# Optimization experiments

Measured on AMD Instinct MI355X. Metric: run time of the kernel, lower is better.

## Reference

```python
import jax, jax.numpy as jnp
import numpy as np

T, B, I, H = 512, 64, 1024, 1024


def setup_inputs() -> dict:
    key = jax.random.key(0)
    ks = jax.random.split(key, 5)
    s = 1.0 / np.sqrt(H)  # torch Linear default init scale
    return {
        "X": jax.random.normal(ks[0], (T, B, I), dtype=jnp.float32),
        "Wi": jax.random.uniform(ks[1], (4, H, I), dtype=jnp.float32, minval=-s, maxval=s),
        "Wh": jax.random.uniform(ks[2], (4, H, H), dtype=jnp.float32, minval=-s, maxval=s),
        "bi": jax.random.uniform(ks[3], (4, H), dtype=jnp.float32, minval=-s, maxval=s),
        "bh": jax.random.uniform(ks[4], (4, H), dtype=jnp.float32, minval=-s, maxval=s),
    }


def _lstm(X, Wi, Wh, bi, bh):
    # Precompute input projections for all timesteps: [T, 4, B, H]
    Gx = jnp.einsum('tbi,ghi->tgbh', X, Wi) + (bi + bh)[None, :, None, :]

    def step(carry, gx):
        h, c = carry
        g = gx + jnp.einsum('ghk,bk->gbh', Wh, h)  # [4, B, H]
        f = jax.nn.sigmoid(g[0])
        i = jax.nn.sigmoid(g[1])
        gg = jnp.tanh(g[2])
        c = f * c + i * gg
        o = jax.nn.sigmoid(g[3])
        h = o * jnp.tanh(c)
        return (h, c), h

    h0 = jnp.zeros((B, H), dtype=X.dtype)
    c0 = jnp.zeros((B, H), dtype=X.dtype)
    (h_n, c_n), outputs = jax.lax.scan(step, (h0, c0), Gx)
    return outputs, h_n[None], c_n[None]  # num_layers=1


def reference(X, Wi, Wh, bi, bh):
    return _lstm(X, Wi, Wh, bi, bh)
```

## Files before the change

### kernel.cpp

```cpp
#include <hip/hip_runtime.h>
#include <hip/hip_bf16.h>

typedef __bf16  bf16_8 __attribute__((ext_vector_type(8)));
typedef short   s16_8  __attribute__((ext_vector_type(8)));
typedef float   f32_4  __attribute__((ext_vector_type(4)));

#define T_ 512

#define LD8(d0,d1,d2,d3,d4,d5,d6,d7, BASE)                                  \
  { unsigned long long _b0 = (BASE), _b1 = (BASE) + 4096ull;                \
    asm volatile(                                                           \
      "global_load_dwordx4 %0, %8, off\n\t"                                 \
      "global_load_dwordx4 %1, %8, off offset:1024\n\t"                     \
      "global_load_dwordx4 %2, %8, off offset:2048\n\t"                     \
      "global_load_dwordx4 %3, %8, off offset:3072\n\t"                     \
      "global_load_dwordx4 %4, %9, off\n\t"                                 \
      "global_load_dwordx4 %5, %9, off offset:1024\n\t"                     \
      "global_load_dwordx4 %6, %9, off offset:2048\n\t"                     \
      "global_load_dwordx4 %7, %9, off offset:3072\n\t"                     \
      : "=&v"(d0),"=&v"(d1),"=&v"(d2),"=&v"(d3),                            \
        "=&v"(d4),"=&v"(d5),"=&v"(d6),"=&v"(d7)                             \
      : "v"(_b0), "v"(_b1)); }

#define LD4C(d0,d1,d2,d3, BASE)                                             \
  { unsigned long long _b0 = (BASE);                                        \
    asm volatile(                                                           \
      "global_load_dwordx4 %0, %4, off sc0 sc1\n\t"                         \
      "global_load_dwordx4 %1, %4, off offset:1024 sc0 sc1\n\t"             \
      "global_load_dwordx4 %2, %4, off offset:2048 sc0 sc1\n\t"             \
      "global_load_dwordx4 %3, %4, off offset:3072 sc0 sc1\n\t"             \
      : "=&v"(d0),"=&v"(d1),"=&v"(d2),"=&v"(d3)                             \
      : "v"(_b0)); }

#define LD32(AF, BASE)                                                      \
  LD8(AF[0][0],AF[0][1],AF[0][2],AF[0][3],AF[0][4],AF[0][5],AF[0][6],AF[0][7], (BASE));          \
  LD8(AF[1][0],AF[1][1],AF[1][2],AF[1][3],AF[1][4],AF[1][5],AF[1][6],AF[1][7], (BASE)+32768ull); \
  LD8(AF[2][0],AF[2][1],AF[2][2],AF[2][3],AF[2][4],AF[2][5],AF[2][6],AF[2][7], (BASE)+65536ull); \
  LD8(AF[3][0],AF[3][1],AF[3][2],AF[3][3],AF[3][4],AF[3][5],AF[3][6],AF[3][7], (BASE)+98304ull);

#define LD16C4(AF, BASE)                                                    \
  LD4C(AF[0][0],AF[0][1],AF[0][2],AF[0][3], (BASE));                        \
  LD4C(AF[1][0],AF[1][1],AF[1][2],AF[1][3], (BASE)+32768ull);               \
  LD4C(AF[2][0],AF[2][1],AF[2][2],AF[2][3], (BASE)+65536ull);               \
  LD4C(AF[3][0],AF[3][1],AF[3][2],AF[3][3], (BASE)+98304ull);

#define VMWAIT_FENCE                                                        \
  asm volatile("s_waitcnt vmcnt(0)" ::: "memory");                          \
  __builtin_amdgcn_sched_barrier(0)

__global__ __launch_bounds__(256) void p1_xfrag(const float* __restrict__ X,
                                                bf16_8* __restrict__ xf) {
  size_t n = (size_t)blockIdx.x * 256 + threadIdx.x;
  int lane = (int)(n & 63);
  int kc   = (int)((n >> 6) & 31);
  int mt   = (int)((n >> 11) & 3);
  int t    = (int)(n >> 13);
  int b  = 16 * mt + (lane & 15);
  int i0 = 32 * kc + (lane >> 4) * 8;
  const float4* ps = (const float4*)(X + ((size_t)t * 64 + b) * 1024 + i0);
  float4 a = ps[0], c = ps[1];
  bf16_8 v;
  v[0]=(__bf16)a.x; v[1]=(__bf16)a.y; v[2]=(__bf16)a.z; v[3]=(__bf16)a.w;
  v[4]=(__bf16)c.x; v[5]=(__bf16)c.y; v[6]=(__bf16)c.z; v[7]=(__bf16)c.w;
  xf[n] = v;
}

__global__ __launch_bounds__(256) void p2_wfrag(const float* __restrict__ Wi,
                                                const float* __restrict__ Wh,
                                                bf16_8* __restrict__ wf) {
  size_t n = (size_t)blockIdx.x * 256 + threadIdx.x;
  int lane = (int)(n & 63);
  int kc   = (int)((n >> 6) & 63);
  int cu   = (int)(n >> 12);
  int n16 = lane & 15;
  int g  = n16 >> 2;
  int jj = n16 & 3;
  int col = 4 * cu + jj;
  int k = 32 * kc + (lane >> 4) * 8;
  const float* src = (k < 1024)
      ? (Wi + ((size_t)g * 1024 + col) * 1024 + k)
      : (Wh + ((size_t)g * 1024 + col) * 1024 + (k - 1024));
  const float4* ps = (const float4*)src;
  float4 a = ps[0], c = ps[1];
  bf16_8 v;
  v[0]=(__bf16)a.x; v[1]=(__bf16)a.y; v[2]=(__bf16)a.z; v[3]=(__bf16)a.w;
  v[4]=(__bf16)c.x; v[5]=(__bf16)c.y; v[6]=(__bf16)c.z; v[7]=(__bf16)c.w;
  wf[n] = v;
}

__global__ __launch_bounds__(512, 2) void lstm_persist(
    const float* __restrict__ bi, const float* __restrict__ bh,
    const s16_8* __restrict__ xfrag, const s16_8* __restrict__ wfrag,
    s16_8* __restrict__ hfrag, float* __restrict__ out,
    unsigned int* __restrict__ ctr)
{
  __shared__ float gx[2][4][64][17];
  __shared__ float gh[8][64][17];
  __shared__ float hvals[2][4][64];
  __shared__ unsigned cell_done;

  const int tid  = threadIdx.x;
  const int cu   = blockIdx.x;
  const int wv   = tid >> 6;
  const int lane = tid & 63;
  const bool ish = (wv >= 4);

  s16_8 whf[4];
#pragma unroll
  for (int i = 0; i < 4; ++i)
    whf[i] = wfrag[((size_t)cu * 64 + 32 + wv * 4 + i) * 64 + lane];
#pragma unroll
  for (int i = 0; i < 4; ++i) asm volatile("" : "+v"(whf[i]));
  s16_8 wxf[8];
  if (!ish) {
#pragma unroll
    for (int i = 0; i < 8; ++i)
      wxf[i] = wfrag[((size_t)cu * 64 + wv * 8 + i) * 64 + lane];
#pragma unroll
    for (int i = 0; i < 8; ++i) asm volatile("" : "+v"(wxf[i]));
  }

  const int et  = tid - 256;
  const int ejj = et & 3;
  const int eb  = et >> 2;
  const int j   = cu * 4 + ejj;
  float bias4[4] = {0.f, 0.f, 0.f, 0.f};
  if (ish) {
#pragma unroll
    for (int g = 0; g < 4; ++g) bias4[g] = bi[g * 1024 + j] + bh[g * 1024 + j];
  }
  float cst = 0.f, hval = 0.f;

  unsigned int* grp = ctr + (cu >> 5) * 64;
  unsigned int* flg = ctr + 1024 + wv * 64;

  if (tid == 0) cell_done = 0u;

  if (!ish) {
    s16_8 af[4][8];
    LD32(af, (unsigned long long)(const char*)xfrag
             + (unsigned)(wv * 8192 + lane * 16));
    VMWAIT_FENCE;
    f32_4 acc[4];
#pragma unroll
    for (int mt = 0; mt < 4; ++mt) { f32_4 z = {0.f,0.f,0.f,0.f}; acc[mt] = z; }
#pragma unroll
    for (int i = 0; i < 8; ++i)
#pragma unroll
      for (int mt = 0; mt < 4; ++mt)
        acc[mt] = __builtin_amdgcn_mfma_f32_16x16x32_bf16(af[mt][i], wxf[i], acc[mt], 0, 0, 0);
#pragma unroll
    for (int mt = 0; mt < 4; ++mt)
#pragma unroll
      for (int r = 0; r < 4; ++r)
        gx[0][wv][mt * 16 + (lane >> 4) * 4 + r][lane & 15] = acc[mt][r];
  }
  __syncthreads();

  for (int t = 0; t < T_; ++t) {
    if (t > 0) {
      if (lane == 0) {
        while (__hip_atomic_load(flg, __ATOMIC_RELAXED, __HIP_MEMORY_SCOPE_AGENT)
               < (unsigned)t) {}
      }
      __builtin_amdgcn_sched_barrier(0);
    }
    {
      s16_8 af[4][4];
      LD16C4(af, (unsigned long long)((const char*)hfrag + (size_t)(t & 1) * 131072)
                 + (unsigned)(wv * 4096 + lane * 16));
      VMWAIT_FENCE;
      f32_4 acc[4];
#pragma unroll
      for (int mt = 0; mt < 4; ++mt) { f32_4 z = {0.f,0.f,0.f,0.f}; acc[mt] = z; }
#pragma unroll
      for (int i = 0; i < 4; ++i)
#pragma unroll
        for (int mt = 0; mt < 4; ++mt)
          acc[mt] = __builtin_amdgcn_mfma_f32_16x16x32_bf16(af[mt][i], whf[i], acc[mt], 0, 0, 0);
#pragma unroll
      for (int mt = 0; mt < 4; ++mt)
#pragma unroll
        for (int r = 0; r < 4; ++r)
          gh[wv][mt * 16 + (lane >> 4) * 4 + r][lane & 15] = acc[mt][r];
    }
    __syncthreads();

    if (ish) {
      const int xb = t & 1;
      float g4[4];
#pragma unroll
      for (int g = 0; g < 4; ++g) {
        float s = bias4[g];
        const int row = g * 4 + ejj;
#pragma unroll
        for (int w = 0; w < 4; ++w) s += gx[xb][w][eb][row];
#pragma unroll
        for (int w = 0; w < 8; ++w) s += gh[w][eb][row];
        g4[g] = s;
      }
      float fg = 1.f / (1.f + __expf(-g4[0]));
      float ig = 1.f / (1.f + __expf(-g4[1]));
      float gg = 1.f - 2.f / (__expf(2.f * g4[2]) + 1.f);
      float og = 1.f / (1.f + __expf(-g4[3]));
      cst  = fg * cst + ig * gg;
      hval = og * (1.f - 2.f / (__expf(2.f * cst) + 1.f));
      hvals[t & 1][ejj][eb] = hval;

      if (t + 1 < T_) {
        int base = lane & ~3;
        float p0 = __shfl(hval, base);
        float p1 = __shfl(hval, base + 1);
        float p2 = __shfl(hval, base + 2);
        float p3 = __shfl(hval, base + 3);
        if ((lane & 3) == 0) {
          unsigned long long pk =
              (unsigned long long)__builtin_bit_cast(unsigned short, (__bf16)p0)
            | ((unsigned long long)__builtin_bit_cast(unsigned short, (__bf16)p1) << 16)
            | ((unsigned long long)__builtin_bit_cast(unsigned short, (__bf16)p2) << 32)
            | ((unsigned long long)__builtin_bit_cast(unsigned short, (__bf16)p3) << 48);
          size_t grpi = ((size_t)(((t + 1) & 1) * 4 + (eb >> 4)) * 32 + (cu >> 3)) * 64
                        + (eb & 15) + 16 * ((cu & 7) >> 1);
          unsigned long long* dst =
              (unsigned long long*)((char*)hfrag + grpi * 16 + (cu & 1) * 8);
          __hip_atomic_store(dst, pk, __ATOMIC_RELAXED, __HIP_MEMORY_SCOPE_AGENT);
        }
        asm volatile("s_waitcnt vmcnt(0)" ::: "memory");
        if (lane == 0)
          __hip_atomic_fetch_add(&cell_done, 1u, __ATOMIC_RELAXED,
                                 __HIP_MEMORY_SCOPE_WORKGROUP);
        if (wv == 4 && lane == 0) {
          while (__hip_atomic_load(&cell_done, __ATOMIC_RELAXED,
                                   __HIP_MEMORY_SCOPE_WORKGROUP) < 4u * (unsigned)(t + 1)) {}
          unsigned old = atomicAdd(grp, 1u);
          if (old == 32u * (unsigned)(t + 1) - 1u)
            __hip_atomic_store(ctr + 1024 + (cu >> 5) * 64, (unsigned)(t + 1),
                               __ATOMIC_RELAXED, __HIP_MEMORY_SCOPE_AGENT);
        }
      }
    } else {
      if (t > 0 && lane < 16) {
        const int s = (t - 1) & 1;
        const int row = wv * 16 + lane;
        float4 o4 = make_float4(hvals[s][0][row], hvals[s][1][row],
                                hvals[s][2][row], hvals[s][3][row]);
        *(float4*)(out + ((size_t)(t - 1) * 64 + row) * 1024 + cu * 4) = o4;
      }
      if (t + 1 < T_) {
        s16_8 af[4][8];
        LD32(af, (unsigned long long)((const char*)xfrag + (size_t)(t + 1) * 131072)
                 + (unsigned)(wv * 8192 + lane * 16));
        VMWAIT_FENCE;
        f32_4 acc[4];
#pragma unroll
        for (int mt = 0; mt < 4; ++mt) { f32_4 z = {0.f,0.f,0.f,0.f}; acc[mt] = z; }
#pragma unroll
        for (int i = 0; i < 8; ++i)
#pragma unroll
          for (int mt = 0; mt < 4; ++mt)
            acc[mt] = __builtin_amdgcn_mfma_f32_16x16x32_bf16(af[mt][i], wxf[i], acc[mt], 0, 0, 0);
#pragma unroll
        for (int mt = 0; mt < 4; ++mt)
#pragma unroll
          for (int r = 0; r < 4; ++r)
            gx[(t + 1) & 1][wv][mt * 16 + (lane >> 4) * 4 + r][lane & 15] = acc[mt][r];
      }
    }
  }

  __syncthreads();
  if (!ish && lane < 16) {
    const int row = wv * 16 + lane;
    float4 o4 = make_float4(hvals[1][0][row], hvals[1][1][row],
                            hvals[1][2][row], hvals[1][3][row]);
    *(float4*)(out + ((size_t)(T_ - 1) * 64 + row) * 1024 + cu * 4) = o4;
  }
  if (ish) {
    out[(size_t)T_ * 65536 + (size_t)eb * 1024 + j] = hval;
    out[(size_t)T_ * 65536 + 65536 + (size_t)eb * 1024 + j] = cst;
  }
}

extern "C" void kernel_launch(void* const* d_in, const int* in_sizes, int n_in,
                              void* d_out, int out_size, void* d_ws, size_t ws_size,
                              hipStream_t stream) {
  (void)in_sizes; (void)n_in;
  const float* X  = (const float*)d_in[0];
  const float* Wi = (const float*)d_in[1];
  const float* Wh = (const float*)d_in[2];
  const float* bi = (const float*)d_in[3];
  const float* bh = (const float*)d_in[4];
  float* out = (float*)d_out;

  char* ws = (char*)d_ws;
  const size_t W_BYTES = (size_t)256 * 64 * 64 * 8 * 2;
  const size_t H_BYTES = (size_t)2 * 4 * 32 * 64 * 8 * 2;
  const size_t C_BYTES = 8192;
  const size_t X_BYTES = (size_t)512 * 4 * 32 * 64 * 8 * 2;

  bf16_8* wfrag = (bf16_8*)ws;
  bf16_8* hfrag = (bf16_8*)(ws + W_BYTES);
  unsigned int* ctr = (unsigned int*)(ws + W_BYTES + H_BYTES);

  bf16_8* xfrag;
  if (ws_size >= W_BYTES + H_BYTES + C_BYTES + X_BYTES) {
    xfrag = (bf16_8*)(ws + W_BYTES + H_BYTES + C_BYTES);
  } else {
    size_t out_bytes = (size_t)out_size * 4;
    xfrag = (bf16_8*)((char*)d_out + out_bytes - X_BYTES);
  }

  hipMemsetAsync(hfrag, 0, 131072, stream);
  hipMemsetAsync(ctr, 0, C_BYTES, stream);

  hipLaunchKernelGGL(p1_xfrag, dim3(16384), dim3(256), 0, stream, X, xfrag);
  hipLaunchKernelGGL(p2_wfrag, dim3(4096), dim3(256), 0, stream, Wi, Wh, wfrag);
  hipLaunchKernelGGL(lstm_persist, dim3(256), dim3(512), 0, stream,
                     bi, bh, (const s16_8*)xfrag, (const s16_8*)wfrag,
                     (s16_8*)hfrag, out, ctr);
}
```

Before: 2.224 ms.

## Split batch across block pairs, widen each block to eight hidden columns

Instead of each block owning 4 hidden units for all 64 batch rows, blocks are paired by batch half (S) and each owns 8 hidden units for 32 batch rows. The weight fragment layout is reordered so each block loads two N-tiles, and the sync uses 16 per-half group counters plus a cross-half lag check. The intent is to halve the per-step h-fragment reads per block and to shrink the synchronization groups while keeping MFMA work per block similar. In exchange each block holds twice the weight registers, and the new cross-half flag wait adds coupling between the two halves.

```diff
diff --git a/kernel.cpp b/kernel.cpp
--- a/kernel.cpp
+++ b/kernel.cpp
@@ -31,18 +31,6 @@
       "global_load_dwordx4 %3, %4, off offset:3072 sc0 sc1\n\t"             \
       : "=&v"(d0),"=&v"(d1),"=&v"(d2),"=&v"(d3)                             \
       : "v"(_b0)); }
-
-#define LD32(AF, BASE)                                                      \
-  LD8(AF[0][0],AF[0][1],AF[0][2],AF[0][3],AF[0][4],AF[0][5],AF[0][6],AF[0][7], (BASE));          \
-  LD8(AF[1][0],AF[1][1],AF[1][2],AF[1][3],AF[1][4],AF[1][5],AF[1][6],AF[1][7], (BASE)+32768ull); \
-  LD8(AF[2][0],AF[2][1],AF[2][2],AF[2][3],AF[2][4],AF[2][5],AF[2][6],AF[2][7], (BASE)+65536ull); \
-  LD8(AF[3][0],AF[3][1],AF[3][2],AF[3][3],AF[3][4],AF[3][5],AF[3][6],AF[3][7], (BASE)+98304ull);
-
-#define LD16C4(AF, BASE)                                                    \
-  LD4C(AF[0][0],AF[0][1],AF[0][2],AF[0][3], (BASE));                        \
-  LD4C(AF[1][0],AF[1][1],AF[1][2],AF[1][3], (BASE)+32768ull);               \
-  LD4C(AF[2][0],AF[2][1],AF[2][2],AF[2][3], (BASE)+65536ull);               \
-  LD4C(AF[3][0],AF[3][1],AF[3][2],AF[3][3], (BASE)+98304ull);
 
 #define VMWAIT_FENCE                                                        \
   asm volatile("s_waitcnt vmcnt(0)" ::: "memory");                          \
@@ -71,20 +59,20 @@
   size_t n = (size_t)blockIdx.x * 256 + threadIdx.x;
   int lane = (int)(n & 63);
   int kc   = (int)((n >> 6) & 63);
-  int cu   = (int)(n >> 12);
+  int nt   = (int)((n >> 12) & 1);
+  int c    = (int)(n >> 13);
   int n16 = lane & 15;
-  int g  = n16 >> 2;
-  int jj = n16 & 3;
-  int col = 4 * cu + jj;
+  int g   = 2 * nt + (n16 >> 3);
+  int col = c * 8 + (n16 & 7);
   int k = 32 * kc + (lane >> 4) * 8;
   const float* src = (k < 1024)
       ? (Wi + ((size_t)g * 1024 + col) * 1024 + k)
       : (Wh + ((size_t)g * 1024 + col) * 1024 + (k - 1024));
   const float4* ps = (const float4*)src;
-  float4 a = ps[0], c = ps[1];
+  float4 a = ps[0], cc = ps[1];
   bf16_8 v;
   v[0]=(__bf16)a.x; v[1]=(__bf16)a.y; v[2]=(__bf16)a.z; v[3]=(__bf16)a.w;
-  v[4]=(__bf16)c.x; v[5]=(__bf16)c.y; v[6]=(__bf16)c.z; v[7]=(__bf16)c.w;
+  v[4]=(__bf16)cc.x; v[5]=(__bf16)cc.y; v[6]=(__bf16)cc.z; v[7]=(__bf16)cc.w;
   wf[n] = v;
 }
 
@@ -94,66 +82,86 @@
     s16_8* __restrict__ hfrag, float* __restrict__ out,
     unsigned int* __restrict__ ctr)
 {
-  __shared__ float gx[2][4][64][17];
-  __shared__ float gh[8][64][17];
-  __shared__ float hvals[2][4][64];
+  __shared__ float gx[2][4][32][33];
+  __shared__ float gh[8][32][33];
+  __shared__ float hvals[2][32][9];
   __shared__ unsigned cell_done;
 
   const int tid  = threadIdx.x;
-  const int cu   = blockIdx.x;
+  const int bid  = blockIdx.x;
+  const int S    = bid & 1;
+  const int c    = bid >> 1;
   const int wv   = tid >> 6;
   const int lane = tid & 63;
   const bool ish = (wv >= 4);
 
-  s16_8 whf[4];
-#pragma unroll
-  for (int i = 0; i < 4; ++i)
-    whf[i] = wfrag[((size_t)cu * 64 + 32 + wv * 4 + i) * 64 + lane];
-#pragma unroll
-  for (int i = 0; i < 4; ++i) asm volatile("" : "+v"(whf[i]));
-  s16_8 wxf[8];
+  s16_8 whf[2][4];
+#pragma unroll
+  for (int nt = 0; nt < 2; ++nt)
+#pragma unroll
+    for (int i = 0; i < 4; ++i)
+      whf[nt][i] = wfrag[(((size_t)c * 2 + nt) * 64 + 32 + wv * 4 + i) * 64 + lane];
+#pragma unroll
+  for (int nt = 0; nt < 2; ++nt)
+#pragma unroll
+    for (int i = 0; i < 4; ++i) asm volatile("" : "+v"(whf[nt][i]));
+  s16_8 wxf[2][8];
   if (!ish) {
 #pragma unroll
-    for (int i = 0; i < 8; ++i)
-      wxf[i] = wfrag[((size_t)cu * 64 + wv * 8 + i) * 64 + lane];
-#pragma unroll
-    for (int i = 0; i < 8; ++i) asm volatile("" : "+v"(wxf[i]));
-  }
-
-  const int et  = tid - 256;
-  const int ejj = et & 3;
-  const int eb  = et >> 2;
-  const int j   = cu * 4 + ejj;
+    for (int nt = 0; nt < 2; ++nt)
+#pragma unroll
+      for (int i = 0; i < 8; ++i)
+        wxf[nt][i] = wfrag[(((size_t)c * 2 + nt) * 64 + wv * 8 + i) * 64 + lane];
+#pragma unroll
+    for (int nt = 0; nt < 2; ++nt)
+#pragma unroll
+      for (int i = 0; i < 8; ++i) asm volatile("" : "+v"(wxf[nt][i]));
+  }
+
+  const int et = tid - 256;
+  const int eq = et & 7;
+  const int eb = et >> 3;
   float bias4[4] = {0.f, 0.f, 0.f, 0.f};
   if (ish) {
 #pragma unroll
-    for (int g = 0; g < 4; ++g) bias4[g] = bi[g * 1024 + j] + bh[g * 1024 + j];
+    for (int g = 0; g < 4; ++g)
+      bias4[g] = bi[g * 1024 + c * 8 + eq] + bh[g * 1024 + c * 8 + eq];
   }
   float cst = 0.f, hval = 0.f;
 
-  unsigned int* grp = ctr + (cu >> 5) * 64;
-  unsigned int* flg = ctr + 1024 + wv * 64;
+  const int gi = S * 8 + (c >> 4);
+  unsigned int* grp   = ctr + gi * 64;
+  unsigned int* flg   = ctr + 1024 + (S * 8 + wv) * 64;
+  unsigned int* oflg  = ctr + 1024 + ((1 - S) * 8 + wv) * 64;
 
   if (tid == 0) cell_done = 0u;
 
   if (!ish) {
-    s16_8 af[4][8];
-    LD32(af, (unsigned long long)(const char*)xfrag
-             + (unsigned)(wv * 8192 + lane * 16));
+    s16_8 af[2][8];
+    unsigned long long xb0 = (unsigned long long)(const char*)xfrag
+        + (unsigned)((2 * S) * 32768 + wv * 8192 + lane * 16);
+    LD8(af[0][0],af[0][1],af[0][2],af[0][3],af[0][4],af[0][5],af[0][6],af[0][7], xb0);
+    LD8(af[1][0],af[1][1],af[1][2],af[1][3],af[1][4],af[1][5],af[1][6],af[1][7], xb0 + 32768ull);
     VMWAIT_FENCE;
-    f32_4 acc[4];
-#pragma unroll
-    for (int mt = 0; mt < 4; ++mt) { f32_4 z = {0.f,0.f,0.f,0.f}; acc[mt] = z; }
+    f32_4 acc[2][2];
+#pragma unroll
+    for (int m = 0; m < 2; ++m)
+#pragma unroll
+      for (int nt = 0; nt < 2; ++nt) { f32_4 z = {0.f,0.f,0.f,0.f}; acc[m][nt] = z; }
 #pragma unroll
     for (int i = 0; i < 8; ++i)
 #pragma unroll
-      for (int mt = 0; mt < 4; ++mt)
-        acc[mt] = __builtin_amdgcn_mfma_f32_16x16x32_bf16(af[mt][i], wxf[i], acc[mt], 0, 0, 0);
-#pragma unroll
-    for (int mt = 0; mt < 4; ++mt)
-#pragma unroll
-      for (int r = 0; r < 4; ++r)
-        gx[0][wv][mt * 16 + (lane >> 4) * 4 + r][lane & 15] = acc[mt][r];
+      for (int m = 0; m < 2; ++m)
+#pragma unroll
+        for (int nt = 0; nt < 2; ++nt)
+          acc[m][nt] = __builtin_amdgcn_mfma_f32_16x16x32_bf16(af[m][i], wxf[nt][i], acc[m][nt], 0, 0, 0);
+#pragma unroll
+    for (int m = 0; m < 2; ++m)
+#pragma unroll
+      for (int nt = 0; nt < 2; ++nt)
+#pragma unroll
+        for (int r = 0; r < 4; ++r)
+          gx[0][wv][m * 16 + (lane >> 4) * 4 + r][nt * 16 + (lane & 15)] = acc[m][nt][r];
   }
   __syncthreads();
 
@@ -163,26 +171,39 @@
         while (__hip_atomic_load(flg, __ATOMIC_RELAXED, __HIP_MEMORY_SCOPE_AGENT)
                < (unsigned)t) {}
       }
+      if (lane == 1 && t > 2) {
+        while (__hip_atomic_load(oflg, __ATOMIC_RELAXED, __HIP_MEMORY_SCOPE_AGENT)
+               < (unsigned)(t - 2)) {}
+      }
       __builtin_amdgcn_sched_barrier(0);
     }
     {
-      s16_8 af[4][4];
-      LD16C4(af, (unsigned long long)((const char*)hfrag + (size_t)(t & 1) * 131072)
-                 + (unsigned)(wv * 4096 + lane * 16));
+      s16_8 af[2][4];
+      unsigned long long hb = (unsigned long long)((const char*)hfrag
+          + (size_t)(t & 1) * 131072)
+          + (unsigned)((2 * S) * 32768 + wv * 4096 + lane * 16);
+      LD4C(af[0][0],af[0][1],af[0][2],af[0][3], hb);
+      LD4C(af[1][0],af[1][1],af[1][2],af[1][3], hb + 32768ull);
       VMWAIT_FENCE;
-      f32_4 acc[4];
-#pragma unroll
-      for (int mt = 0; mt < 4; ++mt) { f32_4 z = {0.f,0.f,0.f,0.f}; acc[mt] = z; }
+      f32_4 acc[2][2];
+#pragma unroll
+      for (int m = 0; m < 2; ++m)
+#pragma unroll
+        for (int nt = 0; nt < 2; ++nt) { f32_4 z = {0.f,0.f,0.f,0.f}; acc[m][nt] = z; }
 #pragma unroll
       for (int i = 0; i < 4; ++i)
 #pragma unroll
-        for (int mt = 0; mt < 4; ++mt)
-          acc[mt] = __builtin_amdgcn_mfma_f32_16x16x32_bf16(af[mt][i], whf[i], acc[mt], 0, 0, 0);
-#pragma unroll
-      for (int mt = 0; mt < 4; ++mt)
-#pragma unroll
-        for (int r = 0; r < 4; ++r)
-          gh[wv][mt * 16 + (lane >> 4) * 4 + r][lane & 15] = acc[mt][r];
+        for (int m = 0; m < 2; ++m)
+#pragma unroll
+          for (int nt = 0; nt < 2; ++nt)
+            acc[m][nt] = __builtin_amdgcn_mfma_f32_16x16x32_bf16(af[m][i], whf[nt][i], acc[m][nt], 0, 0, 0);
+#pragma unroll
+      for (int m = 0; m < 2; ++m)
+#pragma unroll
+        for (int nt = 0; nt < 2; ++nt)
+#pragma unroll
+          for (int r = 0; r < 4; ++r)
+            gh[wv][m * 16 + (lane >> 4) * 4 + r][nt * 16 + (lane & 15)] = acc[m][nt][r];
     }
     __syncthreads();
 
@@ -191,8 +212,8 @@
       float g4[4];
 #pragma unroll
       for (int g = 0; g < 4; ++g) {
+        const int row = g * 8 + eq;
         float s = bias4[g];
-        const int row = g * 4 + ejj;
 #pragma unroll
         for (int w = 0; w < 4; ++w) s += gx[xb][w][eb][row];
 #pragma unroll
@@ -205,25 +226,32 @@
       float og = 1.f / (1.f + __expf(-g4[3]));
       cst  = fg * cst + ig * gg;
       hval = og * (1.f - 2.f / (__expf(2.f * cst) + 1.f));
-      hvals[t & 1][ejj][eb] = hval;
+      hvals[t & 1][eb][eq] = hval;
 
       if (t + 1 < T_) {
-        int base = lane & ~3;
-        float p0 = __shfl(hval, base);
-        float p1 = __shfl(hval, base + 1);
-        float p2 = __shfl(hval, base + 2);
-        float p3 = __shfl(hval, base + 3);
-        if ((lane & 3) == 0) {
-          unsigned long long pk =
+        int base = lane & ~7;
+        float p0 = __shfl(hval, base),     p1 = __shfl(hval, base + 1);
+        float p2 = __shfl(hval, base + 2), p3 = __shfl(hval, base + 3);
+        float p4 = __shfl(hval, base + 4), p5 = __shfl(hval, base + 5);
+        float p6 = __shfl(hval, base + 6), p7 = __shfl(hval, base + 7);
+        if ((lane & 7) == 0) {
+          unsigned long long pk0 =
               (unsigned long long)__builtin_bit_cast(unsigned short, (__bf16)p0)
             | ((unsigned long long)__builtin_bit_cast(unsigned short, (__bf16)p1) << 16)
             | ((unsigned long long)__builtin_bit_cast(unsigned short, (__bf16)p2) << 32)
             | ((unsigned long long)__builtin_bit_cast(unsigned short, (__bf16)p3) << 48);
-          size_t grpi = ((size_t)(((t + 1) & 1) * 4 + (eb >> 4)) * 32 + (cu >> 3)) * 64
-                        + (eb & 15) + 16 * ((cu & 7) >> 1);
-          unsigned long long* dst =
-              (unsigned long long*)((char*)hfrag + grpi * 16 + (cu & 1) * 8);
-          __hip_atomic_store(dst, pk, __ATOMIC_RELAXED, __HIP_MEMORY_SCOPE_AGENT);
+          unsigned long long pk1 =
+              (unsigned long long)__builtin_bit_cast(unsigned short, (__bf16)p4)
+            | ((unsigned long long)__builtin_bit_cast(unsigned short, (__bf16)p5) << 16)
+            | ((unsigned long long)__builtin_bit_cast(unsigned short, (__bf16)p6) << 32)
+            | ((unsigned long long)__builtin_bit_cast(unsigned short, (__bf16)p7) << 48);
+          const int mt = 2 * S + (eb >> 4);
+          size_t b16 = ((size_t)(mt * 32 + (c >> 2)) * 64
+                        + (c & 3) * 16 + (eb & 15)) * 16;
+          unsigned long long* dst = (unsigned long long*)
+              ((char*)hfrag + (size_t)((t + 1) & 1) * 131072 + b16);
+          __hip_atomic_store(dst,     pk0, __ATOMIC_RELAXED, __HIP_MEMORY_SCOPE_AGENT);
+          __hip_atomic_store(dst + 1, pk1, __ATOMIC_RELAXED, __HIP_MEMORY_SCOPE_AGENT);
         }
         asm volatile("s_waitcnt vmcnt(0)" ::: "memory");
         if (lane == 0)
@@ -233,51 +261,62 @@
           while (__hip_atomic_load(&cell_done, __ATOMIC_RELAXED,
                                    __HIP_MEMORY_SCOPE_WORKGROUP) < 4u * (unsigned)(t + 1)) {}
           unsigned old = atomicAdd(grp, 1u);
-          if (old == 32u * (unsigned)(t + 1) - 1u)
-            __hip_atomic_store(ctr + 1024 + (cu >> 5) * 64, (unsigned)(t + 1),
+          if (old == 16u * (unsigned)(t + 1) - 1u)
+            __hip_atomic_store(ctr + 1024 + gi * 64, (unsigned)(t + 1),
                                __ATOMIC_RELAXED, __HIP_MEMORY_SCOPE_AGENT);
         }
       }
     } else {
       if (t > 0 && lane < 16) {
         const int s = (t - 1) & 1;
-        const int row = wv * 16 + lane;
-        float4 o4 = make_float4(hvals[s][0][row], hvals[s][1][row],
-                                hvals[s][2][row], hvals[s][3][row]);
-        *(float4*)(out + ((size_t)(t - 1) * 64 + row) * 1024 + cu * 4) = o4;
+        const int b2 = wv * 8 + (lane >> 1);
+        const int q0 = (lane & 1) * 4;
+        float4 o4 = make_float4(hvals[s][b2][q0],     hvals[s][b2][q0 + 1],
+                                hvals[s][b2][q0 + 2], hvals[s][b2][q0 + 3]);
+        *(float4*)(out + ((size_t)(t - 1) * 64 + 32 * S + b2) * 1024 + c * 8 + q0) = o4;
       }
       if (t + 1 < T_) {
-        s16_8 af[4][8];
-        LD32(af, (unsigned long long)((const char*)xfrag + (size_t)(t + 1) * 131072)
-                 + (unsigned)(wv * 8192 + lane * 16));
+        s16_8 af[2][8];
+        unsigned long long xb0 = (unsigned long long)((const char*)xfrag
+            + (size_t)(t + 1) * 131072)
+            + (unsigned)((2 * S) * 32768 + wv * 8192 + lane * 16);
+        LD8(af[0][0],af[0][1],af[0][2],af[0][3],af[0][4],af[0][5],af[0][6],af[0][7], xb0);
+        LD8(af[1][0],af[1][1],af[1][2],af[1][3],af[1][4],af[1][5],af[1][6],af[1][7], xb0 + 32768ull);
         VMWAIT_FENCE;
-        f32_4 acc[4];
-#pragma unroll
-        for (int mt = 0; mt < 4; ++mt) { f32_4 z = {0.f,0.f,0.f,0.f}; acc[mt] = z; }
+        f32_4 acc[2][2];
+#pragma unroll
+        for (int m = 0; m < 2; ++m)
+#pragma unroll
+          for (int nt = 0; nt < 2; ++nt) { f32_4 z = {0.f,0.f,0.f,0.f}; acc[m][nt] = z; }
 #pragma unroll
         for (int i = 0; i < 8; ++i)
 #pragma unroll
-          for (int mt = 0; mt < 4; ++mt)
-            acc[mt] = __builtin_amdgcn_mfma_f32_16x16x32_bf16(af[mt][i], wxf[i], acc[mt], 0, 0, 0);
-#pragma unroll
-        for (int mt = 0; mt < 4; ++mt)
-#pragma unroll
-          for (int r = 0; r < 4; ++r)
-            gx[(t + 1) & 1][wv][mt * 16 + (lane >> 4) * 4 + r][lane & 15] = acc[mt][r];
+          for (int m = 0; m < 2; ++m)
+#pragma unroll
+            for (int nt = 0; nt < 2; ++nt)
+              acc[m][nt] = __builtin_amdgcn_mfma_f32_16x16x32_bf16(af[m][i], wxf[nt][i], acc[m][nt], 0, 0, 0);
+#pragma unroll
+        for (int m = 0; m < 2; ++m)
+#pragma unroll
+          for (int nt = 0; nt < 2; ++nt)
+#pragma unroll
+            for (int r = 0; r < 4; ++r)
+              gx[(t + 1) & 1][wv][m * 16 + (lane >> 4) * 4 + r][nt * 16 + (lane & 15)] = acc[m][nt][r];
       }
     }
   }
 
   __syncthreads();
   if (!ish && lane < 16) {
-    const int row = wv * 16 + lane;
-    float4 o4 = make_float4(hvals[1][0][row], hvals[1][1][row],
-                            hvals[1][2][row], hvals[1][3][row]);
-    *(float4*)(out + ((size_t)(T_ - 1) * 64 + row) * 1024 + cu * 4) = o4;
+    const int b2 = wv * 8 + (lane >> 1);
+    const int q0 = (lane & 1) * 4;
+    float4 o4 = make_float4(hvals[1][b2][q0],     hvals[1][b2][q0 + 1],
+                            hvals[1][b2][q0 + 2], hvals[1][b2][q0 + 3]);
+    *(float4*)(out + ((size_t)(T_ - 1) * 64 + 32 * S + b2) * 1024 + c * 8 + q0) = o4;
   }
   if (ish) {
-    out[(size_t)T_ * 65536 + (size_t)eb * 1024 + j] = hval;
-    out[(size_t)T_ * 65536 + 65536 + (size_t)eb * 1024 + j] = cst;
+    out[(size_t)T_ * 65536 + (size_t)(32 * S + eb) * 1024 + c * 8 + eq] = hval;
+    out[(size_t)T_ * 65536 + 65536 + (size_t)(32 * S + eb) * 1024 + c * 8 + eq] = cst;
   }
 }
 
@@ -293,9 +332,9 @@
   float* out = (float*)d_out;
 
   char* ws = (char*)d_ws;
-  const size_t W_BYTES = (size_t)256 * 64 * 64 * 8 * 2;
+  const size_t W_BYTES = (size_t)128 * 2 * 64 * 64 * 8 * 2;
   const size_t H_BYTES = (size_t)2 * 4 * 32 * 64 * 8 * 2;
-  const size_t C_BYTES = 8192;
+  const size_t C_BYTES = 16384;
   const size_t X_BYTES = (size_t)512 * 4 * 32 * 64 * 8 * 2;
 
   bf16_8* wfrag = (bf16_8*)ws;
```

New measurement: 2.130 ms. 1.04x faster.
